# Kernel tuning notes

Hardware: AMD Instinct MI355X
Metric: run time of the kernel (lower is better)

The kernel has to match this reference:

```python
import jax, jax.numpy as jnp
import numpy as np

N = 100_000      # num_nodes
E = 1_600_000    # num_edges (avg degree 16)
D = 64           # embedding_dim
L = 3            # num_layers


def setup_inputs() -> dict:
    key = jax.random.key(0)
    k1, k2 = jax.random.split(key)
    edge_index = jax.random.randint(k1, (2, E), 0, N, dtype=jnp.int64)
    edge_weight = jnp.ones((E,), jnp.float32)
    # nn.init.normal_(std=0.1)
    embedding = 0.1 * jax.random.normal(k2, (N, D), dtype=jnp.float32)
    return {"embedding": embedding, "edge_weight": edge_weight, "edge_index": edge_index}


def reference(embedding, edge_weight, edge_index):
    n = embedding.shape[0]
    self_idx = jnp.arange(n, dtype=edge_index.dtype)
    # add_self_loops: append (i, i) with weight 1 (PyG default fill_value)
    row = jnp.concatenate([edge_index[0], self_idx])  # source j
    col = jnp.concatenate([edge_index[1], self_idx])  # target i
    ew = jnp.concatenate([edge_weight, jnp.ones((n,), embedding.dtype)])
    # degree() counts occurrences of row (unweighted)
    deg = jax.ops.segment_sum(jnp.ones_like(ew), row, num_segments=n)
    deg_inv_sqrt = jnp.where(deg > 0, jax.lax.rsqrt(deg), 0.0)
    norm = deg_inv_sqrt[row] * ew * deg_inv_sqrt[col]  # [E+N]

    x = embedding
    acc = embedding  # running sum of layer-0..L embeddings
    for _ in range(L):
        # gather from source, scale, scatter-add to target (dropout off in eval)
        msg = norm[:, None] * x[row]                       # [E+N, D]
        x = jax.ops.segment_sum(msg, col, num_segments=n)  # [N, D]
        acc = acc + x
    return acc / (L + 1)
```

## Files before the change

### kernel.cpp

```cpp
#include <hip/hip_runtime.h>
#include <stdint.h>

#define DIM 64
#define GB 128
#define GSH 7
#define CH 4096
#define TB1 512
#define BINS2 50000
#define RANGES 2
#define NSLICE 64
#define TBH 1024

__device__ __forceinline__ unsigned bf16rne(float f) {
    unsigned u = __float_as_uint(f);
    return (u + 0x7FFFu + ((u >> 16) & 1u)) >> 16;
}
__device__ __forceinline__ unsigned pack2(float lo, float hi) {
    return bf16rne(lo) | (bf16rne(hi) << 16);
}
#define UNPK(u, lo, hi) { lo = __uint_as_float((u) << 16); hi = __uint_as_float((u) & 0xFFFF0000u); }

__global__ void __launch_bounds__(TBH)
hist_src_kernel(const int* __restrict__ src, const int* __restrict__ dst,
                unsigned short* __restrict__ partials, int* __restrict__ bcnt,
                int E, int N, int Es, int NB) {
    __shared__ unsigned h32[BINS2 / 2];
    __shared__ int hb[1024];
    const int b = blockIdx.x;
    const int r = b / NSLICE, s = b % NSLICE;
    const int base = r * BINS2;
    const int hi = min(base + BINS2, N);
    const int nbw = (hi - base + 1) >> 1;
    for (int j = threadIdx.x; j < nbw; j += TBH) h32[j] = 0;
    if (r == 0) for (int j = threadIdx.x; j < NB; j += TBH) hb[j] = 0;
    __syncthreads();
    const int e0 = s * Es, e1 = min(e0 + Es, E);
    if (r == 0) {
#pragma unroll 4
        for (int i = e0 + threadIdx.x; i < e1; i += TBH) {
            unsigned j = (unsigned)(src[i] - base);
            if (j < (unsigned)BINS2) atomicAdd(&h32[j >> 1], 1u << ((j & 1) * 16));
            atomicAdd(&hb[((unsigned)dst[i]) >> GSH], 1);
        }
    } else {
#pragma unroll 4
        for (int i = e0 + threadIdx.x; i < e1; i += TBH) {
            unsigned j = (unsigned)(src[i] - base);
            if (j < (unsigned)BINS2) atomicAdd(&h32[j >> 1], 1u << ((j & 1) * 16));
        }
    }
    __syncthreads();
    unsigned* part = (unsigned*)(partials + (size_t)s * N + base);
    for (int j = threadIdx.x; j < nbw; j += TBH) part[j] = h32[j];
    if (r == 0)
        for (int j = threadIdx.x; j < NB; j += TBH)
            if (hb[j]) atomicAdd(&bcnt[j], hb[j]);
}

__global__ void __launch_bounds__(256)
merge_dis_kernel(const unsigned short* __restrict__ partials, float* __restrict__ dis, int N) {
    const int i = blockIdx.x * blockDim.x + threadIdx.x;
    if (i >= N) return;
    int od = 0;
    for (int s = 0; s < NSLICE; ++s) od += partials[(size_t)s * N + i];
    dis[i] = rsqrtf((float)od + 1.0f);
}

__global__ void scan_buckets(const int* __restrict__ bcnt, int* __restrict__ bucket_base,
                             int* __restrict__ cursor, int* __restrict__ offsets,
                             int NB, int N) {
    __shared__ int buf[1024];
    const int t = threadIdx.x;
    int v = (t < NB) ? bcnt[t] : 0;
    buf[t] = v;
    __syncthreads();
    for (int off = 1; off < 1024; off <<= 1) {
        int add = (t >= off) ? buf[t - off] : 0;
        __syncthreads();
        buf[t] += add;
        __syncthreads();
    }
    if (t < NB) { bucket_base[t] = buf[t] - v; cursor[t] = buf[t] - v; }
    if (t == NB - 1) { bucket_base[NB] = buf[t]; offsets[N] = buf[t]; }
}

__global__ void __launch_bounds__(TB1)
part_kernel(const int* __restrict__ src, const int* __restrict__ dst,
            const float* __restrict__ ew,
            int* __restrict__ cursor, int2* __restrict__ staged, int E, int NB) {
    __shared__ int h[1024];
    const int tid = threadIdx.x;
    const int e0 = blockIdx.x * CH;
    const int e1 = min(e0 + CH, E);
    for (int j = tid; j < NB; j += TB1) h[j] = 0;
    __syncthreads();
    int4 d[CH / (TB1 * 4)];
    int ngrp = 0;
    for (int i = e0 + tid * 4, k = 0; i < e1; i += TB1 * 4, ++k) {
        int4 t;
        if (i + 3 < e1) t = *(const int4*)(dst + i);
        else {
            t.x = dst[i];
            t.y = (i + 1 < e1) ? dst[i + 1] : -1;
            t.z = (i + 2 < e1) ? dst[i + 2] : -1;
            t.w = (i + 3 < e1) ? dst[i + 3] : -1;
        }
        d[k] = t;
        if (t.x >= 0) atomicAdd(&h[t.x >> GSH], 1);
        if (t.y >= 0) atomicAdd(&h[t.y >> GSH], 1);
        if (t.z >= 0) atomicAdd(&h[t.z >> GSH], 1);
        if (t.w >= 0) atomicAdd(&h[t.w >> GSH], 1);
        ngrp = k + 1;
    }
    __syncthreads();
    for (int j = tid; j < NB; j += TB1) {
        int c = h[j];
        h[j] = c ? atomicAdd(&cursor[j], c) : 0;
    }
    __syncthreads();
    for (int i = e0 + tid * 4, k = 0; k < ngrp; i += TB1 * 4, ++k) {
        int4 t = d[k];
        int4 ss = make_int4(0, 0, 0, 0);
        float4 ww = make_float4(0.f, 0.f, 0.f, 0.f);
        if (i + 3 < e1) { ss = *(const int4*)(src + i); ww = *(const float4*)(ew + i); }
        else {
            ss.x = src[i]; ww.x = ew[i];
            if (i + 1 < e1) { ss.y = src[i + 1]; ww.y = ew[i + 1]; }
            if (i + 2 < e1) { ss.z = src[i + 2]; ww.z = ew[i + 2]; }
            if (i + 3 < e1) { ss.w = src[i + 3]; ww.w = ew[i + 3]; }
        }
#define PART1(T, S, W) if ((T) >= 0) { \
        int pos_ = atomicAdd(&h[(T) >> GSH], 1); \
        staged[pos_] = make_int2((S) | (((T) & (GB - 1)) << 20), __float_as_int(W)); }
        PART1(t.x, ss.x, ww.x)
        PART1(t.y, ss.y, ww.y)
        PART1(t.z, ss.z, ww.z)
        PART1(t.w, ss.w, ww.w)
#undef PART1
    }
}

__global__ void __launch_bounds__(256)
place_kernel(const int2* __restrict__ staged, const int* __restrict__ bucket_base,
             const float* __restrict__ dis,
             int* __restrict__ offsets, int2* __restrict__ csr, int N) {
    __shared__ int cnt[GB];
    __shared__ int cur[GB];
    __shared__ int pre[GB + 1];
    __shared__ float disb[GB];
    const int b = blockIdx.x;
    const int n0 = b << GSH;
    const int nb = min(GB, N - n0);
    const int r0 = bucket_base[b], r1 = bucket_base[b + 1];
    for (int j = threadIdx.x; j < GB; j += 256) cnt[j] = 0;
    for (int j = threadIdx.x; j < nb; j += 256) disb[j] = dis[n0 + j];
    __syncthreads();
    for (int i = r0 + threadIdx.x; i < r1; i += 256)
        atomicAdd(&cnt[(staged[i].x >> 20) & (GB - 1)], 1);
    __syncthreads();
    if (threadIdx.x == 0) {
        int run = r0;
        for (int j = 0; j < nb; ++j) { pre[j] = run; run += cnt[j]; }
        pre[nb] = run;
    }
    __syncthreads();
    for (int j = threadIdx.x; j < nb; j += 256) { offsets[n0 + j] = pre[j]; cur[j] = pre[j]; }
    __syncthreads();
    for (int i = r0 + threadIdx.x; i < r1; i += 256) {
        int2 rec = staged[i];
        int tl = (rec.x >> 20) & (GB - 1);
        int s = rec.x & 0xFFFFF;
        int rank = atomicAdd(&cur[tl], 1);
        float w = dis[s] * __int_as_float(rec.y) * disb[tl];
        csr[rank] = make_int2(s, __float_as_int(w));
    }
}

__global__ void __launch_bounds__(256)
conv_kernel(const float4* __restrict__ in4, uint4* __restrict__ outb, int n8) {
    int i = blockIdx.x * blockDim.x + threadIdx.x;
    if (i >= n8) return;
    float4 a = in4[2 * i], b = in4[2 * i + 1];
    uint4 o;
    o.x = pack2(a.x, a.y); o.y = pack2(a.z, a.w);
    o.z = pack2(b.x, b.y); o.w = pack2(b.z, b.w);
    outb[i] = o;
}

__global__ void __launch_bounds__(256)
prop_kernel(const uint4* __restrict__ xg, const float4* __restrict__ selfF,
            uint4* __restrict__ xstore,
            const int* __restrict__ offsets, const int2* __restrict__ csr,
            const float* __restrict__ dis, int n,
            const float4* __restrict__ embF, const uint4* __restrict__ xaF,
            float4* __restrict__ outF) {
    const int lane = threadIdx.x & 63;
    const int fl  = lane & 7;
    const int sub = lane >> 3;
    const int wave = blockIdx.x * (blockDim.x >> 6) + (threadIdx.x >> 6);
    const int node = wave * 8 + sub;
    if (node >= n) return;

    const int beg = offsets[node];
    const int end = offsets[node + 1];
    const float d = dis[node];
    const float dd = d * d;

    float a0, a1, a2, a3, a4, a5, a6, a7;
    uint4 qs = make_uint4(0, 0, 0, 0);
    if (selfF) {
        float4 s0 = selfF[(size_t)node * 16 + fl * 2];
        float4 s1 = selfF[(size_t)node * 16 + fl * 2 + 1];
        a0 = dd * s0.x; a1 = dd * s0.y; a2 = dd * s0.z; a3 = dd * s0.w;
        a4 = dd * s1.x; a5 = dd * s1.y; a6 = dd * s1.z; a7 = dd * s1.w;
    } else {
        qs = xg[(size_t)node * 8 + fl];
        float l, h;
        UNPK(qs.x, l, h) a0 = dd * l; a1 = dd * h;
        UNPK(qs.y, l, h) a2 = dd * l; a3 = dd * h;
        UNPK(qs.z, l, h) a4 = dd * l; a5 = dd * h;
        UNPK(qs.w, l, h) a6 = dd * l; a7 = dd * h;
    }

#define EDGE(E, Q) { float w_ = __int_as_float((E).y); float l, h; \
    UNPK((Q).x, l, h) a0 = fmaf(w_, l, a0); a1 = fmaf(w_, h, a1); \
    UNPK((Q).y, l, h) a2 = fmaf(w_, l, a2); a3 = fmaf(w_, h, a3); \
    UNPK((Q).z, l, h) a4 = fmaf(w_, l, a4); a5 = fmaf(w_, h, a5); \
    UNPK((Q).w, l, h) a6 = fmaf(w_, l, a6); a7 = fmaf(w_, h, a7); }

    int p = beg;
    for (; p + 8 <= end; p += 8) {
        int2 e0 = csr[p + 0], e1 = csr[p + 1], e2 = csr[p + 2], e3 = csr[p + 3];
        int2 e4 = csr[p + 4], e5 = csr[p + 5], e6 = csr[p + 6], e7 = csr[p + 7];
        uint4 q0 = xg[(size_t)e0.x * 8 + fl];
        uint4 q1 = xg[(size_t)e1.x * 8 + fl];
        uint4 q2 = xg[(size_t)e2.x * 8 + fl];
        uint4 q3 = xg[(size_t)e3.x * 8 + fl];
        uint4 q4 = xg[(size_t)e4.x * 8 + fl];
        uint4 q5 = xg[(size_t)e5.x * 8 + fl];
        uint4 q6 = xg[(size_t)e6.x * 8 + fl];
        uint4 q7 = xg[(size_t)e7.x * 8 + fl];
        EDGE(e0, q0) EDGE(e1, q1) EDGE(e2, q2) EDGE(e3, q3)
        EDGE(e4, q4) EDGE(e5, q5) EDGE(e6, q6) EDGE(e7, q7)
    }
    for (; p + 4 <= end; p += 4) {
        int2 e0 = csr[p + 0], e1 = csr[p + 1], e2 = csr[p + 2], e3 = csr[p + 3];
        uint4 q0 = xg[(size_t)e0.x * 8 + fl];
        uint4 q1 = xg[(size_t)e1.x * 8 + fl];
        uint4 q2 = xg[(size_t)e2.x * 8 + fl];
        uint4 q3 = xg[(size_t)e3.x * 8 + fl];
        EDGE(e0, q0) EDGE(e1, q1) EDGE(e2, q2) EDGE(e3, q3)
    }
    for (; p < end; ++p) {
        int2 e = csr[p];
        uint4 q = xg[(size_t)e.x * 8 + fl];
        EDGE(e, q)
    }
#undef EDGE

    if (outF) {
        float4 eA = embF[(size_t)node * 16 + fl * 2];
        float4 eB = embF[(size_t)node * 16 + fl * 2 + 1];
        uint4 qa = xaF[(size_t)node * 8 + fl];
        float r0 = eA.x + a0, r1 = eA.y + a1, r2 = eA.z + a2, r3 = eA.w + a3;
        float r4 = eB.x + a4, r5 = eB.y + a5, r6 = eB.z + a6, r7 = eB.w + a7;
        float l, h;
        UNPK(qa.x, l, h) r0 += l; r1 += h;
        UNPK(qa.y, l, h) r2 += l; r3 += h;
        UNPK(qa.z, l, h) r4 += l; r5 += h;
        UNPK(qa.w, l, h) r6 += l; r7 += h;
        UNPK(qs.x, l, h) r0 += l; r1 += h;
        UNPK(qs.y, l, h) r2 += l; r3 += h;
        UNPK(qs.z, l, h) r4 += l; r5 += h;
        UNPK(qs.w, l, h) r6 += l; r7 += h;
        outF[(size_t)node * 16 + fl * 2] =
            make_float4(0.25f * r0, 0.25f * r1, 0.25f * r2, 0.25f * r3);
        outF[(size_t)node * 16 + fl * 2 + 1] =
            make_float4(0.25f * r4, 0.25f * r5, 0.25f * r6, 0.25f * r7);
    } else {
        uint4 o;
        o.x = pack2(a0, a1); o.y = pack2(a2, a3);
        o.z = pack2(a4, a5); o.w = pack2(a6, a7);
        xstore[(size_t)node * 8 + fl] = o;
    }
}


extern "C" void kernel_launch(void* const* d_in, const int* in_sizes, int n_in,
                              void* d_out, int out_size, void* d_ws, size_t ws_size,
                              hipStream_t stream) {
    const float* emb = (const float*)d_in[0];
    const float* ew  = (const float*)d_in[1];
    const int*   ei  = (const int*)d_in[2];
    const int E = in_sizes[2] / 2;
    const int N = in_sizes[0] / DIM;
    const int* src = ei;
    const int* dst = ei + E;
    float* out = (float*)d_out;

    const int NB = (N + GB - 1) >> GSH;
    const int Es = (E + NSLICE - 1) / NSLICE;

    char* w = (char*)d_ws;
    size_t xSz = ((size_t)N * DIM * 2 + 255) & ~(size_t)255;
    size_t sSz = ((size_t)E * 8 + 255) & ~(size_t)255;
    size_t pSz = ((size_t)NSLICE * N * 2 + 255) & ~(size_t)255;
    size_t uSz = xSz > sSz ? xSz : sSz; if (pSz > uSz) uSz = pSz;
    unsigned short* partials = (unsigned short*)w;
    int2* staged = (int2*)w;
    uint4* xb    = (uint4*)w; w += uSz;
    int2* csr    = (int2*)w; w += sSz;
    uint4* x0c   = (uint4*)w; w += xSz;
    uint4* xa    = (uint4*)w; w += xSz;
    int* offsets = (int*)w; w += ((size_t)(N + 1) * 4 + 255) & ~(size_t)255;
    float* dis   = (float*)w; w += ((size_t)N * 4 + 255) & ~(size_t)255;
    int* bcnt        = (int*)w; w += 1024 * 4;
    int* bucket_base = (int*)w; w += 1025 * 4;
    int* cursor      = (int*)w; w += 1024 * 4;

    const int TB = 256;
    hipMemsetAsync(bcnt, 0, (size_t)NB * 4, stream);

    hist_src_kernel<<<RANGES * NSLICE, TBH, 0, stream>>>(src, dst, partials, bcnt,
                                                         E, N, Es, NB);
    merge_dis_kernel<<<(N + TB - 1) / TB, TB, 0, stream>>>(partials, dis, N);
    scan_buckets<<<1, 1024, 0, stream>>>(bcnt, bucket_base, cursor, offsets, NB, N);
    part_kernel<<<(E + CH - 1) / CH, TB1, 0, stream>>>(src, dst, ew, cursor,
                                                       staged, E, NB);
    place_kernel<<<NB, TB, 0, stream>>>(staged, bucket_base, dis, offsets, csr, N);

    const int n8 = N * DIM / 8;
    conv_kernel<<<(n8 + TB - 1) / TB, TB, 0, stream>>>((const float4*)emb, x0c, n8);

    dim3 grid((N + 31) / 32), block(TB);
    prop_kernel<<<grid, block, 0, stream>>>(x0c, (const float4*)emb, xa,
                                            offsets, csr, dis, N,
                                            nullptr, nullptr, nullptr);
    prop_kernel<<<grid, block, 0, stream>>>(xa, nullptr, xb,
                                            offsets, csr, dis, N,
                                            nullptr, nullptr, nullptr);
    prop_kernel<<<grid, block, 0, stream>>>(xb, nullptr, nullptr,
                                            offsets, csr, dis, N,
                                            (const float4*)emb, xa, (float4*)out);
}
```

Measured before the change: 270.2 us.

## Merge degree histograms via global atomics and stage CSR edges through LDS

The per-slice 16-bit partial histograms and the 64-way merge pass are replaced by atomically adding non-zero shared-memory bins into a single global out-degree array, which is zeroed by one memset. This cuts the write and re-read of NSLICE*N partials. The propagation kernel now cooperatively loads each block's contiguous CSR edge range into a shared-memory buffer in chunks, and each node's sub-wave reads its edge entries from LDS instead of global memory. This adds block-level barriers and keeps inactive lanes alive through the loop.

```diff
diff --git a/kernel.cpp b/kernel.cpp
--- a/kernel.cpp
+++ b/kernel.cpp
@@ -10,6 +10,7 @@
 #define RANGES 2
 #define NSLICE 64
 #define TBH 1024
+#define ECAP 1024
 
 __device__ __forceinline__ unsigned bf16rne(float f) {
     unsigned u = __float_as_uint(f);
@@ -22,7 +23,7 @@
 
 __global__ void __launch_bounds__(TBH)
 hist_src_kernel(const int* __restrict__ src, const int* __restrict__ dst,
-                unsigned short* __restrict__ partials, int* __restrict__ bcnt,
+                int* __restrict__ outdeg, int* __restrict__ bcnt,
                 int E, int N, int Es, int NB) {
     __shared__ unsigned h32[BINS2 / 2];
     __shared__ int hb[1024];
@@ -50,20 +51,25 @@
         }
     }
     __syncthreads();
-    unsigned* part = (unsigned*)(partials + (size_t)s * N + base);
-    for (int j = threadIdx.x; j < nbw; j += TBH) part[j] = h32[j];
+    for (int j = threadIdx.x; j < nbw; j += TBH) {
+        unsigned v = h32[j];
+        if (v) {
+            unsigned lo = v & 0xFFFFu, hh = v >> 16;
+            int nidx = base + 2 * j;
+            if (lo) atomicAdd((unsigned*)&outdeg[nidx], lo);
+            if (hh && nidx + 1 < N) atomicAdd((unsigned*)&outdeg[nidx + 1], hh);
+        }
+    }
     if (r == 0)
         for (int j = threadIdx.x; j < NB; j += TBH)
             if (hb[j]) atomicAdd(&bcnt[j], hb[j]);
 }
 
 __global__ void __launch_bounds__(256)
-merge_dis_kernel(const unsigned short* __restrict__ partials, float* __restrict__ dis, int N) {
+dis_kernel(const int* __restrict__ outdeg, float* __restrict__ dis, int N) {
     const int i = blockIdx.x * blockDim.x + threadIdx.x;
     if (i >= N) return;
-    int od = 0;
-    for (int s = 0; s < NSLICE; ++s) od += partials[(size_t)s * N + i];
-    dis[i] = rsqrtf((float)od + 1.0f);
+    dis[i] = rsqrtf((float)outdeg[i] + 1.0f);
 }
 
 __global__ void scan_buckets(const int* __restrict__ bcnt, int* __restrict__ bucket_base,
@@ -194,32 +200,43 @@
             const float* __restrict__ dis, int n,
             const float4* __restrict__ embF, const uint4* __restrict__ xaF,
             float4* __restrict__ outF) {
-    const int lane = threadIdx.x & 63;
+    __shared__ int2 elds[ECAP];
+    const int tid = threadIdx.x;
+    const int lane = tid & 63;
     const int fl  = lane & 7;
     const int sub = lane >> 3;
-    const int wave = blockIdx.x * (blockDim.x >> 6) + (threadIdx.x >> 6);
-    const int node = wave * 8 + sub;
-    if (node >= n) return;
-
-    const int beg = offsets[node];
-    const int end = offsets[node + 1];
-    const float d = dis[node];
+    const int node0 = blockIdx.x * 32;
+    const int nodeL = min(node0 + 32, n);
+    const int gbeg = offsets[node0];
+    const int gend = offsets[nodeL];
+
+    const int node = node0 + (tid >> 6) * 8 + sub;
+    const bool active = (node < n);
+    int beg = gbeg, end = gbeg;
+    float d = 0.f;
+    if (active) {
+        beg = offsets[node];
+        end = offsets[node + 1];
+        d = dis[node];
+    }
     const float dd = d * d;
 
-    float a0, a1, a2, a3, a4, a5, a6, a7;
+    float a0 = 0, a1 = 0, a2 = 0, a3 = 0, a4 = 0, a5 = 0, a6 = 0, a7 = 0;
     uint4 qs = make_uint4(0, 0, 0, 0);
-    if (selfF) {
-        float4 s0 = selfF[(size_t)node * 16 + fl * 2];
-        float4 s1 = selfF[(size_t)node * 16 + fl * 2 + 1];
-        a0 = dd * s0.x; a1 = dd * s0.y; a2 = dd * s0.z; a3 = dd * s0.w;
-        a4 = dd * s1.x; a5 = dd * s1.y; a6 = dd * s1.z; a7 = dd * s1.w;
-    } else {
-        qs = xg[(size_t)node * 8 + fl];
-        float l, h;
-        UNPK(qs.x, l, h) a0 = dd * l; a1 = dd * h;
-        UNPK(qs.y, l, h) a2 = dd * l; a3 = dd * h;
-        UNPK(qs.z, l, h) a4 = dd * l; a5 = dd * h;
-        UNPK(qs.w, l, h) a6 = dd * l; a7 = dd * h;
+    if (active) {
+        if (selfF) {
+            float4 s0 = selfF[(size_t)node * 16 + fl * 2];
+            float4 s1 = selfF[(size_t)node * 16 + fl * 2 + 1];
+            a0 = dd * s0.x; a1 = dd * s0.y; a2 = dd * s0.z; a3 = dd * s0.w;
+            a4 = dd * s1.x; a5 = dd * s1.y; a6 = dd * s1.z; a7 = dd * s1.w;
+        } else {
+            qs = xg[(size_t)node * 8 + fl];
+            float l, h;
+            UNPK(qs.x, l, h) a0 = dd * l; a1 = dd * h;
+            UNPK(qs.y, l, h) a2 = dd * l; a3 = dd * h;
+            UNPK(qs.z, l, h) a4 = dd * l; a5 = dd * h;
+            UNPK(qs.w, l, h) a6 = dd * l; a7 = dd * h;
+        }
     }
 
 #define EDGE(E, Q) { float w_ = __int_as_float((E).y); float l, h; \
@@ -228,36 +245,46 @@
     UNPK((Q).z, l, h) a4 = fmaf(w_, l, a4); a5 = fmaf(w_, h, a5); \
     UNPK((Q).w, l, h) a6 = fmaf(w_, l, a6); a7 = fmaf(w_, h, a7); }
 
-    int p = beg;
-    for (; p + 8 <= end; p += 8) {
-        int2 e0 = csr[p + 0], e1 = csr[p + 1], e2 = csr[p + 2], e3 = csr[p + 3];
-        int2 e4 = csr[p + 4], e5 = csr[p + 5], e6 = csr[p + 6], e7 = csr[p + 7];
-        uint4 q0 = xg[(size_t)e0.x * 8 + fl];
-        uint4 q1 = xg[(size_t)e1.x * 8 + fl];
-        uint4 q2 = xg[(size_t)e2.x * 8 + fl];
-        uint4 q3 = xg[(size_t)e3.x * 8 + fl];
-        uint4 q4 = xg[(size_t)e4.x * 8 + fl];
-        uint4 q5 = xg[(size_t)e5.x * 8 + fl];
-        uint4 q6 = xg[(size_t)e6.x * 8 + fl];
-        uint4 q7 = xg[(size_t)e7.x * 8 + fl];
-        EDGE(e0, q0) EDGE(e1, q1) EDGE(e2, q2) EDGE(e3, q3)
-        EDGE(e4, q4) EDGE(e5, q5) EDGE(e6, q6) EDGE(e7, q7)
-    }
-    for (; p + 4 <= end; p += 4) {
-        int2 e0 = csr[p + 0], e1 = csr[p + 1], e2 = csr[p + 2], e3 = csr[p + 3];
-        uint4 q0 = xg[(size_t)e0.x * 8 + fl];
-        uint4 q1 = xg[(size_t)e1.x * 8 + fl];
-        uint4 q2 = xg[(size_t)e2.x * 8 + fl];
-        uint4 q3 = xg[(size_t)e3.x * 8 + fl];
-        EDGE(e0, q0) EDGE(e1, q1) EDGE(e2, q2) EDGE(e3, q3)
-    }
-    for (; p < end; ++p) {
-        int2 e = csr[p];
-        uint4 q = xg[(size_t)e.x * 8 + fl];
-        EDGE(e, q)
+    for (int c0 = gbeg; c0 < gend; c0 += ECAP) {
+        const int c1 = min(c0 + ECAP, gend);
+        __syncthreads();
+        for (int i = tid; i < c1 - c0; i += 256) elds[i] = csr[c0 + i];
+        __syncthreads();
+        int p  = (beg > c0) ? beg : c0;
+        const int pe = (end < c1) ? end : c1;
+        for (; p + 8 <= pe; p += 8) {
+            const int q = p - c0;
+            int2 e0 = elds[q + 0], e1 = elds[q + 1], e2 = elds[q + 2], e3 = elds[q + 3];
+            int2 e4 = elds[q + 4], e5 = elds[q + 5], e6 = elds[q + 6], e7 = elds[q + 7];
+            uint4 q0 = xg[(size_t)e0.x * 8 + fl];
+            uint4 q1 = xg[(size_t)e1.x * 8 + fl];
+            uint4 q2 = xg[(size_t)e2.x * 8 + fl];
+            uint4 q3 = xg[(size_t)e3.x * 8 + fl];
+            uint4 q4 = xg[(size_t)e4.x * 8 + fl];
+            uint4 q5 = xg[(size_t)e5.x * 8 + fl];
+            uint4 q6 = xg[(size_t)e6.x * 8 + fl];
+            uint4 q7 = xg[(size_t)e7.x * 8 + fl];
+            EDGE(e0, q0) EDGE(e1, q1) EDGE(e2, q2) EDGE(e3, q3)
+            EDGE(e4, q4) EDGE(e5, q5) EDGE(e6, q6) EDGE(e7, q7)
+        }
+        for (; p + 4 <= pe; p += 4) {
+            const int q = p - c0;
+            int2 e0 = elds[q + 0], e1 = elds[q + 1], e2 = elds[q + 2], e3 = elds[q + 3];
+            uint4 q0 = xg[(size_t)e0.x * 8 + fl];
+            uint4 q1 = xg[(size_t)e1.x * 8 + fl];
+            uint4 q2 = xg[(size_t)e2.x * 8 + fl];
+            uint4 q3 = xg[(size_t)e3.x * 8 + fl];
+            EDGE(e0, q0) EDGE(e1, q1) EDGE(e2, q2) EDGE(e3, q3)
+        }
+        for (; p < pe; ++p) {
+            int2 e = elds[p - c0];
+            uint4 q = xg[(size_t)e.x * 8 + fl];
+            EDGE(e, q)
+        }
     }
 #undef EDGE
 
+    if (!active) return;
     if (outF) {
         float4 eA = embF[(size_t)node * 16 + fl * 2];
         float4 eB = embF[(size_t)node * 16 + fl * 2 + 1];
@@ -304,9 +331,7 @@
     char* w = (char*)d_ws;
     size_t xSz = ((size_t)N * DIM * 2 + 255) & ~(size_t)255;
     size_t sSz = ((size_t)E * 8 + 255) & ~(size_t)255;
-    size_t pSz = ((size_t)NSLICE * N * 2 + 255) & ~(size_t)255;
-    size_t uSz = xSz > sSz ? xSz : sSz; if (pSz > uSz) uSz = pSz;
-    unsigned short* partials = (unsigned short*)w;
+    size_t uSz = xSz > sSz ? xSz : sSz;
     int2* staged = (int2*)w;
     uint4* xb    = (uint4*)w; w += uSz;
     int2* csr    = (int2*)w; w += sSz;
@@ -314,16 +339,18 @@
     uint4* xa    = (uint4*)w; w += xSz;
     int* offsets = (int*)w; w += ((size_t)(N + 1) * 4 + 255) & ~(size_t)255;
     float* dis   = (float*)w; w += ((size_t)N * 4 + 255) & ~(size_t)255;
-    int* bcnt        = (int*)w; w += 1024 * 4;
+    int* outdeg  = (int*)w;
+    int* bcnt    = outdeg + N;
+    w += ((size_t)(N + 1024) * 4 + 255) & ~(size_t)255;
     int* bucket_base = (int*)w; w += 1025 * 4;
     int* cursor      = (int*)w; w += 1024 * 4;
 
     const int TB = 256;
-    hipMemsetAsync(bcnt, 0, (size_t)NB * 4, stream);
-
-    hist_src_kernel<<<RANGES * NSLICE, TBH, 0, stream>>>(src, dst, partials, bcnt,
+    hipMemsetAsync(outdeg, 0, (size_t)(N + 1024) * 4, stream);
+
+    hist_src_kernel<<<RANGES * NSLICE, TBH, 0, stream>>>(src, dst, outdeg, bcnt,
                                                          E, N, Es, NB);
-    merge_dis_kernel<<<(N + TB - 1) / TB, TB, 0, stream>>>(partials, dis, N);
+    dis_kernel<<<(N + TB - 1) / TB, TB, 0, stream>>>(outdeg, dis, N);
     scan_buckets<<<1, 1024, 0, stream>>>(bcnt, bucket_base, cursor, offsets, NB, N);
     part_kernel<<<(E + CH - 1) / CH, TB1, 0, stream>>>(src, dst, ew, cursor,
                                                        staged, E, NB);
```

Measured after the change: 285.7 us. 5.7% more time.
